# Optimization experiments

Hardware: AMD Instinct MI355X
Metric: run time of the kernel (lower is better)

## Reference

```python
import jax, jax.numpy as jnp
import numpy as np

CONF_THRESH = 0.01
TOP_K = 200
NMS_THRESH = 0.45


def setup_inputs() -> dict:
    key = jax.random.key(0)
    k1, k2, k3, k4, k5 = jax.random.split(key, 5)
    B, N, C = 32, 8732, 21
    return {
        "loc_data": jax.random.normal(k1, (B, N, 4), jnp.float32),
        "conf_data": jax.random.normal(k2, (B, N, C), jnp.float32),
        "pose_data": jax.random.normal(k3, (B, N, 32), jnp.float32),
        "line_data": jax.random.normal(k4, (B, N, 3), jnp.float32),
        "dbox_list": jax.random.uniform(k5, (N, 4), jnp.float32),
    }


def decode(loc, dbox):
    # loc, dbox: [N,4]; variances 0.1 / 0.2 as in the torch decode()
    cxcy = dbox[:, :2] + loc[:, :2] * 0.1 * dbox[:, 2:]
    wh = dbox[:, 2:] * jnp.exp(loc[:, 2:] * 0.2)
    mins = cxcy - wh / 2.0
    maxs = mins + wh
    return jnp.concatenate([mins, maxs], axis=1)  # [N,4] xyxy


def nms_class(boxes, scores, poses, lines):
    """Greedy NMS for one (batch, class). boxes [N,4], scores [N] (softmax probs).
    Matches torch nm_suppression: candidates are the top_k by score above
    conf_thresh; suppress IoU > overlap; at most top_k kept."""
    s0 = jnp.where(scores > CONF_THRESH, scores, -jnp.inf)
    _, cand_idx = jax.lax.top_k(s0, TOP_K)  # descending-score candidate pool
    cb = boxes[cand_idx]                     # [K,4]
    cs = s0[cand_idx]                        # [K], -inf where below threshold
    x1, y1, x2, y2 = cb[:, 0], cb[:, 1], cb[:, 2], cb[:, 3]
    area = (x2 - x1) * (y2 - y1)
    K = TOP_K
    ar = jnp.arange(K)

    def step(s, _):
        i = jnp.argmax(s)
        take = jnp.isfinite(s[i])
        xx1 = jnp.maximum(x1, x1[i])
        yy1 = jnp.maximum(y1, y1[i])
        xx2 = jnp.minimum(x2, x2[i])
        yy2 = jnp.minimum(y2, y2[i])
        inter = jnp.clip(xx2 - xx1, 0.0) * jnp.clip(yy2 - yy1, 0.0)
        union = area - inter + area[i]
        iou = inter / union
        supp = (iou > NMS_THRESH) | (ar == i)
        s_new = jnp.where(take & supp, -jnp.inf, s)
        return s_new, (i, take)

    _, (pos, take) = jax.lax.scan(step, cs, None, length=K)
    gi = cand_idx[pos]  # global box indices of kept detections [K]
    row = jnp.concatenate(
        [scores[gi][:, None], boxes[gi], poses[gi], lines[gi]], axis=1
    )  # [K, 1+4+32+3] = [200, 40]
    return row * take[:, None].astype(row.dtype)


def reference(loc_data, conf_data, pose_data, line_data, dbox_list):
    conf = jax.nn.softmax(conf_data, axis=-1)                       # [B,N,C]
    boxes = jax.vmap(decode, in_axes=(0, None))(loc_data, dbox_list)  # [B,N,4]
    per_cls = jax.vmap(nms_class, in_axes=(None, 1, None, None))    # over classes
    per_batch = jax.vmap(per_cls, in_axes=(0, 0, 0, 0))             # over batch
    out = per_batch(boxes, conf, pose_data, line_data)              # [B,C,200,40]
    return out.at[:, 0].set(0.0)  # class 0 (background) is skipped in torch loop
```

## Files before the change

### kernel.cpp

```cpp
#include <hip/hip_runtime.h>
#include <math.h>

#define BB 32
#define NN 8732
#define CC 21
#define TOPK 200
#define NPOSE 32
#define NLINE 3
#define NBINS 2048
#define CAP 1024
#define ROWW 40
#define NT 512

__device__ __forceinline__ double fexp12(double x) {
  const double LOG2E = 1.4426950408889634074;
  const double LN2HI = 6.93147180369123816490e-01;
  const double LN2LO = 1.90821492927058770002e-10;
  double kd = rint(x * LOG2E);
  double r = fma(-kd, LN2HI, x);
  r = fma(-kd, LN2LO, r);
  double p = 2.08767569878680989792e-09;
  p = fma(p, r, 2.50521083854417187751e-08);
  p = fma(p, r, 2.75573192239858906526e-07);
  p = fma(p, r, 2.75573192239858925110e-06);
  p = fma(p, r, 2.48015873015873015873e-05);
  p = fma(p, r, 1.98412698412698412698e-04);
  p = fma(p, r, 1.38888888888888888889e-03);
  p = fma(p, r, 8.33333333333333333333e-03);
  p = fma(p, r, 4.16666666666666666667e-02);
  p = fma(p, r, 1.66666666666666666667e-01);
  p = fma(p, r, 0.5);
  p = fma(p, r, 1.0);
  p = fma(p, r, 1.0);
  int k = (int)kd;
  k = k < -1020 ? -1020 : (k > 1020 ? 1020 : k);
  double sc = __longlong_as_double((long long)(1023 + k) << 52);
  return p * sc;
}

__device__ __forceinline__ double fexp_t(double x, const double* __restrict__ T) {
  const double INV64 = 1.4426950408889634074 * 64.0;
  const double L64HI = 6.93147180369123816490e-01 / 64.0;
  const double L64LO = 1.90821492927058770002e-10 / 64.0;
  double kd = rint(x * INV64);
  double r = fma(-kd, L64HI, x);
  r = fma(-kd, L64LO, r);
  double p = 4.16666666666666666667e-02;
  p = fma(p, r, 1.66666666666666666667e-01);
  p = fma(p, r, 0.5);
  p = fma(p, r, 1.0);
  p = fma(p, r, 1.0);
  int ki = (int)kd;
  double t = T[ki & 63];
  int e = ki >> 6;
  e = e < -1020 ? -1020 : e;
  double sc = __longlong_as_double((long long)(1023 + e) << 52);
  return (t * p) * sc;
}

__global__ __launch_bounds__(256, 4) void score_kernel(
    const float* __restrict__ conf, float* __restrict__ scores) {
  __shared__ __align__(16) float buf[256 * CC];
  __shared__ double Texp[64];
  const int tid = threadIdx.x;
  const int i0 = blockIdx.x * 256;
  const int base = i0 * CC;
  int total = BB * NN * CC - base;
  if (total > 256 * CC) total = 256 * CC;
  {
    const float4* g4 = (const float4*)(conf + base);
    float4* b4 = (float4*)buf;
    const int n4 = total >> 2;
    for (int t = tid; t < n4; t += 256) b4[t] = g4[t];
  }
  if (tid < 64)
    Texp[tid] = fexp12((double)tid * (6.93147180369123816490e-01 / 64.0));
  __syncthreads();
  const int i = i0 + tid;
  if (i >= BB * NN) return;
  const float* p = buf + tid * CC;
  float x[CC];
#pragma unroll
  for (int c = 0; c < CC; ++c) x[c] = p[c];
  float m = x[0];
#pragma unroll
  for (int c = 1; c < CC; ++c) m = fmaxf(m, x[c]);
  float e[CC];
#pragma unroll
  for (int c = 0; c < CC; ++c) e[c] = (float)fexp_t((double)(x[c] - m), Texp);
  float r0 = e[0] + e[8], r1 = e[1] + e[9], r2 = e[2] + e[10], r3 = e[3] + e[11];
  float r4 = e[4] + e[12], r5 = e[5] + e[13], r6 = e[6] + e[14], r7 = e[7] + e[15];
  float sum = ((r0 + r1) + (r2 + r3)) + ((r4 + r5) + (r6 + r7));
  sum += e[16]; sum += e[17]; sum += e[18]; sum += e[19]; sum += e[20];
  const int b = i / NN, n = i - b * NN;
#pragma unroll
  for (int c = 0; c < CC; ++c)
    scores[((size_t)b * CC + c) * NN + n] = e[c] / sum;
}

__device__ __forceinline__ int score_bin(float s) {
  unsigned u = __float_as_uint(s);
  int bin = (int)(u >> 15) - 30720;
  return bin < 0 ? 0 : (bin > NBINS - 1 ? NBINS - 1 : bin);
}

__device__ __forceinline__ float score_full(const float* conf, int b, int c, int n) {
  const float* p = conf + ((size_t)b * NN + n) * CC;
  float mm = p[0];
  for (int c2 = 1; c2 < CC; ++c2) mm = fmaxf(mm, p[c2]);
  float e[CC];
  for (int c2 = 0; c2 < CC; ++c2) e[c2] = (float)fexp12((double)(p[c2] - mm));
  float r0 = e[0] + e[8], r1 = e[1] + e[9], r2 = e[2] + e[10], r3 = e[3] + e[11];
  float r4 = e[4] + e[12], r5 = e[5] + e[13], r6 = e[6] + e[14], r7 = e[7] + e[15];
  float sum = ((r0 + r1) + (r2 + r3)) + ((r4 + r5) + (r6 + r7));
  sum += e[16]; sum += e[17]; sum += e[18]; sum += e[19]; sum += e[20];
  return e[c] / sum;
}

__global__ __launch_bounds__(NT, 4) void nms_kernel(
    const float* __restrict__ loc, const float* __restrict__ conf,
    const float* __restrict__ pose, const float* __restrict__ line,
    const float* __restrict__ dbox, const float* __restrict__ scores,
    int mode, float* __restrict__ out) {
  const int bc = blockIdx.x;
  const int b = bc / CC, c = bc - b * CC;
  const int tid = threadIdx.x;
  const int wv = tid >> 6, lane = tid & 63;
  float* outSlab = out + (size_t)bc * (TOPK * ROWW);
  const float4 z4 = make_float4(0.f, 0.f, 0.f, 0.f);

  if (c == 0) {
    float4* o4 = (float4*)outSlab;
    for (int i = tid; i < TOPK * ROWW / 4; i += NT) o4[i] = z4;
    return;
  }

  __shared__ int hist[NBINS];
  __shared__ __align__(16) unsigned long long ckey[CAP + 16];
  __shared__ float4 cbox[TOPK];
  __shared__ float sScore[TOPK];
  __shared__ int sIdx[TOPK];
  __shared__ unsigned long long supp[TOPK * 4];
  __shared__ unsigned long long rowAnyBits[4];
  __shared__ int kept[TOPK];
  __shared__ int waveTot[8];
  __shared__ int sBT, sCnt, sKept;

  const float* scoresB = scores + ((size_t)b * CC + c) * NN;

  float4 v[5];
  if (mode == 1) {
#pragma unroll
    for (int k = 0; k < 4; ++k)
      v[k] = *(const float4*)(scoresB + k * 2048 + tid * 4);
    if (tid < 135)
      v[4] = *(const float4*)(scoresB + 8192 + tid * 4);
    else
      v[4] = make_float4(-1.f, -1.f, -1.f, -1.f);
  } else {
#pragma unroll 1
    for (int k = 0; k < 5; ++k) {
      const int n0 = (k < 4 ? k * 2048 : 8192) + (tid << 2);
      if (k < 4 || tid < 135) {
        v[k].x = score_full(conf, b, c, n0 + 0);
        v[k].y = score_full(conf, b, c, n0 + 1);
        v[k].z = score_full(conf, b, c, n0 + 2);
        v[k].w = score_full(conf, b, c, n0 + 3);
      } else {
        v[k] = make_float4(-1.f, -1.f, -1.f, -1.f);
      }
    }
  }

  for (int i = tid; i < NBINS; i += NT) hist[i] = 0;
  if (tid == 0) { sCnt = 0; sBT = 0; }
  __syncthreads();

#pragma unroll
  for (int k = 0; k < 5; ++k) {
    if (v[k].x > 0.01f) atomicAdd(&hist[score_bin(v[k].x)], 1);
    if (v[k].y > 0.01f) atomicAdd(&hist[score_bin(v[k].y)], 1);
    if (v[k].z > 0.01f) atomicAdd(&hist[score_bin(v[k].z)], 1);
    if (v[k].w > 0.01f) atomicAdd(&hist[score_bin(v[k].w)], 1);
  }
  __syncthreads();

  int s4 = hist[tid * 4] + hist[tid * 4 + 1] + hist[tid * 4 + 2] + hist[tid * 4 + 3];
  int cs = s4;
#pragma unroll
  for (int d = 1; d < 64; d <<= 1) {
    int t = __shfl_down(cs, d, 64);
    if (lane + d < 64) cs += t;
  }
  if (lane == 0) waveTot[wv] = cs;
  __syncthreads();
  {
    int higher = 0;
    for (int g = wv + 1; g < 8; ++g) higher += waveTot[g];
    int incl = cs + higher;
    int excl = incl - s4;
    if (excl < TOPK && incl >= TOPK) {
      int cum = excl, bt = tid * 4;
      for (int bin = tid * 4 + 3;; --bin) {
        cum += hist[bin];
        if (cum >= TOPK || bin == tid * 4) { bt = bin; break; }
      }
      sBT = bt;
    }
  }
  __syncthreads();
  const int bt = sBT;

#pragma unroll
  for (int k = 0; k < 5; ++k) {
    float sv[4] = {v[k].x, v[k].y, v[k].z, v[k].w};
#pragma unroll
    for (int j = 0; j < 4; ++j) {
      float s = sv[j];
      if (s > 0.01f && score_bin(s) >= bt) {
        int p = atomicAdd(&sCnt, 1);
        if (p < CAP) {
          unsigned n = (unsigned)((k < 4 ? k * 2048 : 8192) + (tid << 2) + j);
          ckey[p] = ((unsigned long long)__float_as_uint(s) << 32) |
                    (unsigned long long)(0xFFFFFFFFu - n);
        }
      }
    }
  }
  __syncthreads();
  const int M = sCnt < CAP ? sCnt : CAP;
  if (M == 0) {
    float4* o4 = (float4*)outSlab;
    for (int i = tid; i < TOPK * ROWW / 4; i += NT) o4[i] = z4;
    return;
  }
  const int K = M < TOPK ? M : TOPK;
  const int Mpad = (M + 15) & ~15;
  for (int i = M + tid; i < Mpad; i += NT) ckey[i] = 0ull;
  __syncthreads();

  const float* locB = loc + (size_t)b * NN * 4;
  for (int t = tid; t < M; t += NT) {
    unsigned long long kt = ckey[t];
    unsigned n = 0xFFFFFFFFu - (unsigned)(kt & 0xFFFFFFFFull);
    float4 l4 = *(const float4*)(locB + (size_t)n * 4);
    float4 d4 = *(const float4*)(dbox + (size_t)n * 4);
    int r = 0;
    for (int j0 = 0; j0 < Mpad; j0 += 8) {
      ulonglong2 kk[4];
#pragma unroll
      for (int q = 0; q < 4; ++q)
        kk[q] = *(const ulonglong2*)(ckey + j0 + 2 * q);
#pragma unroll
      for (int q = 0; q < 4; ++q) {
        r += (kk[q].x > kt) ? 1 : 0;
        r += (kk[q].y > kt) ? 1 : 0;
      }
    }
    if (r < TOPK) {
      float cx = d4.x + (l4.x * 0.1f) * d4.z;
      float cy = d4.y + (l4.y * 0.1f) * d4.w;
      float w = d4.z * (float)fexp12((double)(l4.z * 0.2f));
      float h = d4.w * (float)fexp12((double)(l4.w * 0.2f));
      float x1 = cx - w * 0.5f;
      float y1 = cy - h * 0.5f;
      float x2 = x1 + w;
      float y2 = y1 + h;
      cbox[r] = make_float4(x1, y1, x2, y2);
      sScore[r] = __uint_as_float((unsigned)(kt >> 32));
      sIdx[r] = (int)n;
    }
  }
  __syncthreads();

  {
    const double TMID = (double)0.45f + 0x1p-26;
    const int lw = wv & 3, half = wv >> 2;
    const int l = lw * 64 + lane;
    const bool lvalid = l < K;
    float4 lb = lvalid ? cbox[l] : z4;
    float lar = (lb.z - lb.x) * (lb.w - lb.y);
    const int jlim = (K < lw * 64 + 63) ? K : (lw * 64 + 63);
    const int jmid = jlim >> 1;
    const int jstart = half ? jmid : 0;
    const int jend = half ? jlim : jmid;
    for (int j0 = jstart; j0 < jend; j0 += 4) {
      const int jc = (jend - j0 < 4) ? (jend - j0) : 4;
      float4 jb[4];
#pragma unroll
      for (int q = 0; q < 4; ++q)
        if (q < jc) jb[q] = cbox[j0 + q];
      unsigned long long mres[4];
#pragma unroll
      for (int q = 0; q < 4; ++q) {
        if (q < jc) {
          float ja = (jb[q].z - jb[q].x) * (jb[q].w - jb[q].y);
          float xx1 = fmaxf(lb.x, jb[q].x);
          float yy1 = fmaxf(lb.y, jb[q].y);
          float xx2 = fminf(lb.z, jb[q].z);
          float yy2 = fminf(lb.w, jb[q].w);
          float iw = fmaxf(xx2 - xx1, 0.0f);
          float ih = fmaxf(yy2 - yy1, 0.0f);
          float inter = iw * ih;
          float uni = (lar - inter) + ja;
          double tt = fma(-TMID, (double)uni, (double)inter);
          bool hit = lvalid & (l > (j0 + q)) & (tt > 0.0);
          mres[q] = __ballot((int)hit);
        }
      }
      if (lane == 0) {
#pragma unroll
        for (int q = 0; q < 4; ++q)
          if (q < jc) supp[(j0 + q) * 4 + lw] = mres[q];
      }
    }
    if (half == 1 && lane == 0)
      for (int j = jlim; j < K; ++j) supp[j * 4 + lw] = 0ull;
  }
  __syncthreads();

  if (tid < 256) {
    bool nz = false;
    if (tid < K)
      nz = (supp[tid * 4 + 0] | supp[tid * 4 + 1] |
            supp[tid * 4 + 2] | supp[tid * 4 + 3]) != 0ull;
    unsigned long long bal = __ballot((int)nz);
    if (lane == 0) rowAnyBits[wv] = bal;
  }
  __syncthreads();

  if (tid == 0) {
    unsigned long long alive[4];
#pragma unroll
    for (int w = 0; w < 4; ++w) {
      int cnt = K - w * 64;
      alive[w] = cnt <= 0 ? 0ull : (cnt >= 64 ? ~0ull : ((1ull << cnt) - 1ull));
    }
    int nk = 0;
#pragma unroll
    for (int w = 0; w < 4; ++w) {
      const unsigned long long raw = rowAnyBits[w];
      while (alive[w]) {
        int bit = __ffsll(alive[w]) - 1;
        int j = w * 64 + bit;
        kept[nk++] = j;
        alive[w] &= ~(1ull << bit);
        if ((raw >> bit) & 1) {
          unsigned long long r0 = supp[j * 4 + 0];
          unsigned long long r1 = supp[j * 4 + 1];
          unsigned long long r2 = supp[j * 4 + 2];
          unsigned long long r3 = supp[j * 4 + 3];
          alive[0] &= ~r0; alive[1] &= ~r1; alive[2] &= ~r2; alive[3] &= ~r3;
        }
      }
    }
    sKept = nk;
  }
  __syncthreads();

  const int nk = sKept;
  const float* poseB = pose + (size_t)b * NN * NPOSE;
  const float* lineB = line + (size_t)b * NN * NLINE;
  for (int t = tid; t < nk; t += NT) {
    int j = kept[t];
    int n = sIdx[j];
    float* row = outSlab + (size_t)t * ROWW;
    float4 bx = cbox[j];
    const float4* p4 = (const float4*)(poseB + (size_t)n * NPOSE);
    float l0 = lineB[(size_t)n * NLINE + 0];
    float l1 = lineB[(size_t)n * NLINE + 1];
    float l2 = lineB[(size_t)n * NLINE + 2];
    row[0] = sScore[j];
    row[1] = bx.x;
    row[2] = bx.y;
    row[3] = bx.z;
    row[4] = bx.w;
#pragma unroll
    for (int q = 0; q < 8; ++q) {
      float4 pv = p4[q];
      row[5 + 4 * q + 0] = pv.x;
      row[5 + 4 * q + 1] = pv.y;
      row[5 + 4 * q + 2] = pv.z;
      row[5 + 4 * q + 3] = pv.w;
    }
    row[37] = l0;
    row[38] = l1;
    row[39] = l2;
  }
  {
    const int zq = (TOPK - nk) * 10;
    float4* o4 = (float4*)(outSlab + (size_t)nk * ROWW);
    for (int q = tid; q < zq; q += NT) o4[q] = z4;
  }
}

extern "C" void kernel_launch(void* const* d_in, const int* in_sizes, int n_in,
                              void* d_out, int out_size, void* d_ws, size_t ws_size,
                              hipStream_t stream) {
  const float* loc  = (const float*)d_in[0];
  const float* conf = (const float*)d_in[1];
  const float* pose = (const float*)d_in[2];
  const float* line = (const float*)d_in[3];
  const float* dbox = (const float*)d_in[4];
  float* out = (float*)d_out;

  const size_t scoreBytes = (size_t)BB * CC * NN * sizeof(float);
  int mode = (ws_size >= scoreBytes) ? 1 : 0;
  float* scores = mode ? (float*)d_ws : nullptr;

  if (mode) {
    const int total = BB * NN;
    score_kernel<<<(total + 255) / 256, 256, 0, stream>>>(conf, scores);
  }
  nms_kernel<<<BB * CC, NT, 0, stream>>>(loc, conf, pose, line, dbox,
                                         scores, mode, out);
}
```

Before: 181.6 us.

## Parallelize greedy NMS scan across a wavefront and spread output gather per element

```diff
diff --git a/kernel.cpp b/kernel.cpp
--- a/kernel.cpp
+++ b/kernel.cpp
@@ -117,6 +117,12 @@
   return e[c] / sum;
 }
 
+__device__ __forceinline__ unsigned long long rl64(unsigned long long v, int sl) {
+  unsigned lo = (unsigned)__builtin_amdgcn_readlane((int)(unsigned)(v & 0xFFFFFFFFull), sl);
+  unsigned hi = (unsigned)__builtin_amdgcn_readlane((int)(unsigned)(v >> 32), sl);
+  return ((unsigned long long)hi << 32) | (unsigned long long)lo;
+}
+
 __global__ __launch_bounds__(NT, 4) void nms_kernel(
     const float* __restrict__ loc, const float* __restrict__ conf,
     const float* __restrict__ pose, const float* __restrict__ line,
@@ -140,8 +146,7 @@
   __shared__ float4 cbox[TOPK];
   __shared__ float sScore[TOPK];
   __shared__ int sIdx[TOPK];
-  __shared__ unsigned long long supp[TOPK * 4];
-  __shared__ unsigned long long rowAnyBits[4];
+  __shared__ __align__(16) unsigned long long supp[TOPK * 4];
   __shared__ int kept[TOPK];
   __shared__ int waveTot[8];
   __shared__ int sBT, sCnt, sKept;
@@ -237,6 +242,11 @@
   const int K = M < TOPK ? M : TOPK;
   const int Mpad = (M + 15) & ~15;
   for (int i = M + tid; i < Mpad; i += NT) ckey[i] = 0ull;
+
+  {
+    float4* o4 = (float4*)outSlab;
+    for (int i = tid; i < TOPK * ROWW / 4; i += NT) o4[i] = z4;
+  }
   __syncthreads();
 
   const float* locB = loc + (size_t)b * NN * 4;
@@ -319,78 +329,78 @@
   }
   __syncthreads();
 
-  if (tid < 256) {
-    bool nz = false;
-    if (tid < K)
-      nz = (supp[tid * 4 + 0] | supp[tid * 4 + 1] |
-            supp[tid * 4 + 2] | supp[tid * 4 + 3]) != 0ull;
-    unsigned long long bal = __ballot((int)nz);
-    if (lane == 0) rowAnyBits[wv] = bal;
-  }
-  __syncthreads();
-
-  if (tid == 0) {
-    unsigned long long alive[4];
-#pragma unroll
-    for (int w = 0; w < 4; ++w) {
-      int cnt = K - w * 64;
-      alive[w] = cnt <= 0 ? 0ull : (cnt >= 64 ? ~0ull : ((1ull << cnt) - 1ull));
-    }
-    int nk = 0;
-#pragma unroll
-    for (int w = 0; w < 4; ++w) {
-      const unsigned long long raw = rowAnyBits[w];
-      while (alive[w]) {
-        int bit = __ffsll(alive[w]) - 1;
-        int j = w * 64 + bit;
-        kept[nk++] = j;
-        alive[w] &= ~(1ull << bit);
-        if ((raw >> bit) & 1) {
-          unsigned long long r0 = supp[j * 4 + 0];
-          unsigned long long r1 = supp[j * 4 + 1];
-          unsigned long long r2 = supp[j * 4 + 2];
-          unsigned long long r3 = supp[j * 4 + 3];
-          alive[0] &= ~r0; alive[1] &= ~r1; alive[2] &= ~r2; alive[3] &= ~r3;
-        }
-      }
-    }
-    sKept = nk;
+  if (wv == 0) {
+    const ulonglong2 zz = make_ulonglong2(0ull, 0ull);
+    const ulonglong2* sp = (const ulonglong2*)supp;
+    const int r0 = lane, r1 = 64 + lane, r2 = 128 + lane, r3 = 192 + lane;
+    ulonglong2 ra01 = (r0 < K) ? sp[r0 * 2] : zz;
+    ulonglong2 ra23 = (r0 < K) ? sp[r0 * 2 + 1] : zz;
+    ulonglong2 rb01 = (r1 < K) ? sp[r1 * 2] : zz;
+    ulonglong2 rb23 = (r1 < K) ? sp[r1 * 2 + 1] : zz;
+    ulonglong2 rc01 = (r2 < K) ? sp[r2 * 2] : zz;
+    ulonglong2 rc23 = (r2 < K) ? sp[r2 * 2 + 1] : zz;
+    ulonglong2 rd01 = (r3 < K) ? sp[r3 * 2] : zz;
+    ulonglong2 rd23 = (r3 < K) ? sp[r3 * 2 + 1] : zz;
+
+    unsigned long long a0, a1, a2, a3;
+    {
+      int c0 = K, c1 = K - 64, c2 = K - 128, c3 = K - 192;
+      a0 = c0 <= 0 ? 0ull : (c0 >= 64 ? ~0ull : ((1ull << c0) - 1ull));
+      a1 = c1 <= 0 ? 0ull : (c1 >= 64 ? ~0ull : ((1ull << c1) - 1ull));
+      a2 = c2 <= 0 ? 0ull : (c2 >= 64 ? ~0ull : ((1ull << c2) - 1ull));
+      a3 = c3 <= 0 ? 0ull : (c3 >= 64 ? ~0ull : ((1ull << c3) - 1ull));
+    }
+    unsigned long long k0 = 0ull, k1 = 0ull, k2 = 0ull, k3 = 0ull;
+
+    while (a0 | a1 | a2 | a3) {
+      int w, sl;
+      if (a0)      { w = 0; sl = __ffsll(a0) - 1; }
+      else if (a1) { w = 1; sl = __ffsll(a1) - 1; }
+      else if (a2) { w = 2; sl = __ffsll(a2) - 1; }
+      else         { w = 3; sl = __ffsll(a3) - 1; }
+      ulonglong2 h01 = (w == 0) ? ra01 : (w == 1) ? rb01 : (w == 2) ? rc01 : rd01;
+      ulonglong2 h23 = (w == 0) ? ra23 : (w == 1) ? rb23 : (w == 2) ? rc23 : rd23;
+      unsigned long long q0 = rl64(h01.x, sl);
+      unsigned long long q1 = rl64(h01.y, sl);
+      unsigned long long q2 = rl64(h23.x, sl);
+      unsigned long long q3 = rl64(h23.y, sl);
+      if (w == 0)      { k0 |= 1ull << sl; a0 &= ~(1ull << sl); }
+      else if (w == 1) { k1 |= 1ull << sl; a1 &= ~(1ull << sl); }
+      else if (w == 2) { k2 |= 1ull << sl; a2 &= ~(1ull << sl); }
+      else             { k3 |= 1ull << sl; a3 &= ~(1ull << sl); }
+      a0 &= ~q0; a1 &= ~q1; a2 &= ~q2; a3 &= ~q3;
+    }
+
+    const unsigned long long lmask = (1ull << lane) - 1ull;
+    const int c0 = __popcll(k0), c1 = __popcll(k1), c2 = __popcll(k2);
+    if ((k0 >> lane) & 1ull) kept[__popcll(k0 & lmask)] = lane;
+    if ((k1 >> lane) & 1ull) kept[c0 + __popcll(k1 & lmask)] = 64 + lane;
+    if ((k2 >> lane) & 1ull) kept[c0 + c1 + __popcll(k2 & lmask)] = 128 + lane;
+    if ((k3 >> lane) & 1ull) kept[c0 + c1 + c2 + __popcll(k3 & lmask)] = 192 + lane;
+    if (lane == 0) sKept = c0 + c1 + c2 + __popcll(k3);
   }
   __syncthreads();
 
   const int nk = sKept;
   const float* poseB = pose + (size_t)b * NN * NPOSE;
   const float* lineB = line + (size_t)b * NN * NLINE;
-  for (int t = tid; t < nk; t += NT) {
-    int j = kept[t];
-    int n = sIdx[j];
-    float* row = outSlab + (size_t)t * ROWW;
-    float4 bx = cbox[j];
-    const float4* p4 = (const float4*)(poseB + (size_t)n * NPOSE);
-    float l0 = lineB[(size_t)n * NLINE + 0];
-    float l1 = lineB[(size_t)n * NLINE + 1];
-    float l2 = lineB[(size_t)n * NLINE + 2];
-    row[0] = sScore[j];
-    row[1] = bx.x;
-    row[2] = bx.y;
-    row[3] = bx.z;
-    row[4] = bx.w;
-#pragma unroll
-    for (int q = 0; q < 8; ++q) {
-      float4 pv = p4[q];
-      row[5 + 4 * q + 0] = pv.x;
-      row[5 + 4 * q + 1] = pv.y;
-      row[5 + 4 * q + 2] = pv.z;
-      row[5 + 4 * q + 3] = pv.w;
-    }
-    row[37] = l0;
-    row[38] = l1;
-    row[39] = l2;
-  }
-  {
-    const int zq = (TOPK - nk) * 10;
-    float4* o4 = (float4*)(outSlab + (size_t)nk * ROWW);
-    for (int q = tid; q < zq; q += NT) o4[q] = z4;
+  const int tot = nk * ROWW;
+  for (int e = tid; e < tot; e += NT) {
+    const int t = e / ROWW;
+    const int ci = e - t * ROWW;
+    const int j = kept[t];
+    float val;
+    if (ci == 0) {
+      val = sScore[j];
+    } else if (ci < 5) {
+      const float4 bx = cbox[j];
+      val = (ci == 1) ? bx.x : (ci == 2) ? bx.y : (ci == 3) ? bx.z : bx.w;
+    } else if (ci < 37) {
+      val = poseB[(size_t)sIdx[j] * NPOSE + (ci - 5)];
+    } else {
+      val = lineB[(size_t)sIdx[j] * NLINE + (ci - 37)];
+    }
+    outSlab[e] = val;
   }
 }
 
```

After: 226.4 us. +24.6%, slower.

## Run greedy NMS scan wave-parallel with readlane and prefetch pose/line rows

Applied to the files above, without the earlier changes.

```diff
diff --git a/kernel.cpp b/kernel.cpp
--- a/kernel.cpp
+++ b/kernel.cpp
@@ -117,6 +117,12 @@
   return e[c] / sum;
 }
 
+__device__ __forceinline__ unsigned long long rl64(unsigned long long v, int sl) {
+  unsigned lo = (unsigned)__builtin_amdgcn_readlane((int)(unsigned)(v & 0xFFFFFFFFull), sl);
+  unsigned hi = (unsigned)__builtin_amdgcn_readlane((int)(unsigned)(v >> 32), sl);
+  return ((unsigned long long)hi << 32) | (unsigned long long)lo;
+}
+
 __global__ __launch_bounds__(NT, 4) void nms_kernel(
     const float* __restrict__ loc, const float* __restrict__ conf,
     const float* __restrict__ pose, const float* __restrict__ line,
@@ -140,13 +146,14 @@
   __shared__ float4 cbox[TOPK];
   __shared__ float sScore[TOPK];
   __shared__ int sIdx[TOPK];
-  __shared__ unsigned long long supp[TOPK * 4];
-  __shared__ unsigned long long rowAnyBits[4];
+  __shared__ __align__(32) unsigned long long supp[TOPK * 4];
   __shared__ int kept[TOPK];
   __shared__ int waveTot[8];
   __shared__ int sBT, sCnt, sKept;
 
   const float* scoresB = scores + ((size_t)b * CC + c) * NN;
+  const float* poseB = pose + (size_t)b * NN * NPOSE;
+  const float* lineB = line + (size_t)b * NN * NLINE;
 
   float4 v[5];
   if (mode == 1) {
@@ -273,6 +280,16 @@
   }
   __syncthreads();
 
+  if (tid < 2 * TOPK) {
+    const int row = tid >> 1;
+    if (row < K) {
+      const int n = sIdx[row];
+      float pp = poseB[(size_t)n * NPOSE + (tid & 1) * 16];
+      float ll = lineB[(size_t)n * NLINE + (tid & 1) * 2];
+      asm volatile("" :: "v"(pp), "v"(ll));
+    }
+  }
+
   {
     const double TMID = (double)0.45f + 0x1p-26;
     const int lw = wv & 3, half = wv >> 2;
@@ -319,48 +336,53 @@
   }
   __syncthreads();
 
-  if (tid < 256) {
-    bool nz = false;
-    if (tid < K)
-      nz = (supp[tid * 4 + 0] | supp[tid * 4 + 1] |
-            supp[tid * 4 + 2] | supp[tid * 4 + 3]) != 0ull;
-    unsigned long long bal = __ballot((int)nz);
-    if (lane == 0) rowAnyBits[wv] = bal;
-  }
-  __syncthreads();
-
-  if (tid == 0) {
-    unsigned long long alive[4];
-#pragma unroll
-    for (int w = 0; w < 4; ++w) {
-      int cnt = K - w * 64;
-      alive[w] = cnt <= 0 ? 0ull : (cnt >= 64 ? ~0ull : ((1ull << cnt) - 1ull));
-    }
-    int nk = 0;
-#pragma unroll
-    for (int w = 0; w < 4; ++w) {
-      const unsigned long long raw = rowAnyBits[w];
-      while (alive[w]) {
-        int bit = __ffsll(alive[w]) - 1;
-        int j = w * 64 + bit;
-        kept[nk++] = j;
-        alive[w] &= ~(1ull << bit);
-        if ((raw >> bit) & 1) {
-          unsigned long long r0 = supp[j * 4 + 0];
-          unsigned long long r1 = supp[j * 4 + 1];
-          unsigned long long r2 = supp[j * 4 + 2];
-          unsigned long long r3 = supp[j * 4 + 3];
-          alive[0] &= ~r0; alive[1] &= ~r1; alive[2] &= ~r2; alive[3] &= ~r3;
-        }
-      }
-    }
-    sKept = nk;
+  if (wv == 0) {
+    unsigned long long a0, a1, a2, a3;
+    {
+      int c0 = K, c1 = K - 64, c2 = K - 128, c3 = K - 192;
+      a0 = c0 <= 0 ? 0ull : (c0 >= 64 ? ~0ull : ((1ull << c0) - 1ull));
+      a1 = c1 <= 0 ? 0ull : (c1 >= 64 ? ~0ull : ((1ull << c1) - 1ull));
+      a2 = c2 <= 0 ? 0ull : (c2 >= 64 ? ~0ull : ((1ull << c2) - 1ull));
+      a3 = c3 <= 0 ? 0ull : (c3 >= 64 ? ~0ull : ((1ull << c3) - 1ull));
+    }
+    unsigned long long k0 = 0ull, k1 = 0ull, k2 = 0ull, k3 = 0ull;
+    const ulonglong2 zz = make_ulonglong2(0ull, 0ull);
+    const ulonglong2* sp = (const ulonglong2*)supp;
+
+#define GREEDY_CHUNK(W, AW, KW)                                              \
+    if (AW) {                                                                \
+      const int r = (W) * 64 + lane;                                         \
+      ulonglong2 s01 = zz, s23 = zz;                                         \
+      if (r < K) { s01 = sp[r * 2]; s23 = sp[r * 2 + 1]; }                   \
+      while (AW) {                                                           \
+        int sl = __ffsll(AW) - 1;                                            \
+        KW |= 1ull << sl;                                                    \
+        AW &= ~(1ull << sl);                                                 \
+        unsigned long long q0 = rl64(s01.x, sl);                             \
+        unsigned long long q1 = rl64(s01.y, sl);                             \
+        unsigned long long q2 = rl64(s23.x, sl);                             \
+        unsigned long long q3 = rl64(s23.y, sl);                             \
+        a0 &= ~q0; a1 &= ~q1; a2 &= ~q2; a3 &= ~q3;                          \
+      }                                                                      \
+    }
+
+    GREEDY_CHUNK(0, a0, k0)
+    GREEDY_CHUNK(1, a1, k1)
+    GREEDY_CHUNK(2, a2, k2)
+    GREEDY_CHUNK(3, a3, k3)
+#undef GREEDY_CHUNK
+
+    const unsigned long long lmask = (1ull << lane) - 1ull;
+    const int c0 = __popcll(k0), c1 = __popcll(k1), c2 = __popcll(k2);
+    if ((k0 >> lane) & 1ull) kept[__popcll(k0 & lmask)] = lane;
+    if ((k1 >> lane) & 1ull) kept[c0 + __popcll(k1 & lmask)] = 64 + lane;
+    if ((k2 >> lane) & 1ull) kept[c0 + c1 + __popcll(k2 & lmask)] = 128 + lane;
+    if ((k3 >> lane) & 1ull) kept[c0 + c1 + c2 + __popcll(k3 & lmask)] = 192 + lane;
+    if (lane == 0) sKept = c0 + c1 + c2 + __popcll(k3);
   }
   __syncthreads();
 
   const int nk = sKept;
-  const float* poseB = pose + (size_t)b * NN * NPOSE;
-  const float* lineB = line + (size_t)b * NN * NLINE;
   for (int t = tid; t < nk; t += NT) {
     int j = kept[t];
     int n = sIdx[j];
```

After: 178.1 us. About the same (-2.0%).
